# Kernel optimization log

Hardware: AMD Instinct MI355X
Metric: run time of the kernel (lower is better)

## Reference

```python
import jax, jax.numpy as jnp
import numpy as np
from jax import lax

B, H, W, CL, CC, CD, NH, NP = 8, 48, 48, 384, 384, 384, 12, 4
N = H * W
HD = CL // NH
SCALE = HD ** -0.5


def _pool_mat(n, out=7):
    # torch AdaptiveAvgPool2d bin edges: [floor(i*n/out), ceil((i+1)*n/out))
    M = np.zeros((out, n), np.float32)
    for i in range(out):
        s = (i * n) // out
        e = -(-((i + 1) * n) // out)
        M[i, s:e] = 1.0 / (e - s)
    return jnp.asarray(M)


def _resize_mat(out_n, in_n):
    # bilinear, align_corners=False (torch F.interpolate)
    M = np.zeros((out_n, in_n), np.float32)
    scale = in_n / out_n
    for o in range(out_n):
        src = (o + 0.5) * scale - 0.5
        src = min(max(src, 0.0), in_n - 1.0)
        i0 = int(np.floor(src))
        i1 = min(i0 + 1, in_n - 1)
        f = src - i0
        M[o, i0] += 1.0 - f
        M[o, i1] += f
    return jnp.asarray(M)


def _ln_c(x, g, b):
    # LayerNorm over channel dim of NCHW, eps=1e-6
    mu = jnp.mean(x, axis=1, keepdims=True)
    var = jnp.mean((x - mu) ** 2, axis=1, keepdims=True)
    xn = (x - mu) * lax.rsqrt(var + 1e-6)
    return xn * g[None, :, None, None] + b[None, :, None, None]


def _c1(x, w):
    # 1x1 conv, w: (out,in)
    return jnp.einsum('oc,bchw->bohw', w, x)


def _bilerp(feat, grid):
    # feat (G,C,Hs,Ws), grid (G,M,2) xy in [-1,1]; align_corners=False, zero padding
    G, C, Hs, Ws = feat.shape
    x = (grid[..., 0] + 1.0) * 0.5 * Ws - 0.5
    y = (grid[..., 1] + 1.0) * 0.5 * Hs - 0.5
    x0 = jnp.floor(x)
    y0 = jnp.floor(y)
    fx = x - x0
    fy = y - y0
    featf = feat.transpose(0, 2, 3, 1).reshape(G, Hs * Ws, C)
    x0i = x0.astype(jnp.int32)
    y0i = y0.astype(jnp.int32)

    def corner(ix, iy):
        valid = ((ix >= 0) & (ix < Ws) & (iy >= 0) & (iy < Hs)).astype(feat.dtype)
        flat = jnp.clip(iy, 0, Hs - 1) * Ws + jnp.clip(ix, 0, Ws - 1)
        g = jax.vmap(lambda f, i: f[i])(featf, flat)  # (G,M,C)
        return g * valid[..., None]

    v00 = corner(x0i, y0i)
    v01 = corner(x0i + 1, y0i)
    v10 = corner(x0i, y0i + 1)
    v11 = corner(x0i + 1, y0i + 1)
    w00 = ((1 - fx) * (1 - fy))[..., None]
    w01 = (fx * (1 - fy))[..., None]
    w10 = ((1 - fx) * fy)[..., None]
    w11 = (fx * fy)[..., None]
    return v00 * w00 + v01 * w01 + v10 * w10 + v11 * w11  # (G,M,C)


def _forward(local_feat, context_prior, deformable_x, W_q, W_k, W_v, W_pre, ln1_g, ln1_b,
             W_post, dw_w, dw_b, ln2_g, ln2_b, W_lo, b_lo, W_off, b_off,
             attention_biases, W_p, bn_g, bn_b, bn_mean, bn_var):
    q = _c1(local_feat, W_q)  # (B,CL,H,W)

    # context_offset_guide: 1x1 -> GELU -> adaptive pool 7x7 -> LN(C) -> 1x1 to 32 -> resize
    cg = jax.nn.gelu(_c1(context_prior, W_pre), approximate=False)
    Mh, Mw = _pool_mat(H), _pool_mat(W)
    pooled = jnp.einsum('oh,pw,bchw->bcop', Mh, Mw, cg)
    guide = _c1(_ln_c(pooled, ln1_g, ln1_b), W_post)  # (B,32,7,7)
    Uh, Uw = _resize_mat(H, 7), _resize_mat(W, 7)
    guide = jnp.einsum('Oh,Pw,bchw->bcOP', Uh, Uw, guide)  # (B,32,H,W)

    # local_offset_base: dwconv3x3 -> LN(C) -> GELU -> 1x1 to 32
    dw = lax.conv_general_dilated(local_feat, dw_w, (1, 1), [(1, 1), (1, 1)],
                                  dimension_numbers=('NCHW', 'OIHW', 'NCHW'),
                                  feature_group_count=CL) + dw_b[None, :, None, None]
    lo = jax.nn.gelu(_ln_c(dw, ln2_g, ln2_b), approximate=False)
    lo = _c1(lo, W_lo) + b_lo[None, :, None, None]  # (B,32,H,W)

    fused = jnp.concatenate([guide, lo], axis=1)  # (B,64,H,W)
    off = _c1(fused, W_off) + b_off[None, :, None, None]  # (B,NH*NP*2,H,W)
    off = off.transpose(0, 2, 3, 1).reshape(B, H, W, NH, NP, 2)
    offn = off / jnp.asarray([W, H], dtype=off.dtype)

    ry = (jnp.arange(H, dtype=off.dtype) + 0.5) / H
    rx = (jnp.arange(W, dtype=off.dtype) + 0.5) / W
    ref = jnp.stack([jnp.broadcast_to(rx[None, :], (H, W)),
                     jnp.broadcast_to(ry[:, None], (H, W))], axis=-1)  # (H,W,2) xy
    grid = (ref[None, :, :, None, None, :] + offn) * 2.0 - 1.0  # (B,H,W,NH,NP,2)

    gridh = grid.reshape(B, N, NH, NP, 2).transpose(0, 2, 1, 3, 4)  # (B,NH,N,NP,2)
    grid_r = gridh.reshape(B * NH, N * NP, 2)

    k = _c1(context_prior, W_k).reshape(B * NH, HD, H, W)
    v = _c1(deformable_x, W_v).reshape(B * NH, HD, H, W)
    k_s = _bilerp(k, grid_r).reshape(B, NH, N, NP, HD)
    v_s = _bilerp(v, grid_r).reshape(B, NH, N, NP, HD)

    qh = q.reshape(B, NH, HD, N).transpose(0, 1, 3, 2)  # (B,NH,N,HD)
    scores = jnp.einsum('bhnd,bhnpd->bhnp', qh, k_s) * SCALE

    # relative position bias: idx(p1,p2) = |dy|*W + |dx| (first-seen enumeration)
    px = jnp.clip(jnp.round((gridh[..., 0] + 1.0) * 0.5 * W - 0.5), 0, W - 1).astype(jnp.int32)
    py = jnp.clip(jnp.round((gridh[..., 1] + 1.0) * 0.5 * H - 0.5), 0, H - 1).astype(jnp.int32)
    n = jnp.arange(N, dtype=jnp.int32)
    qy = (n // W)[None, None, :, None]
    qx = (n % W)[None, None, :, None]
    bidx = jnp.abs(qy - py) * W + jnp.abs(qx - px)  # (B,NH,N,NP)
    bias = attention_biases[jnp.arange(NH)[None, :, None, None], bidx]

    attn = jax.nn.softmax(scores + bias, axis=-1)
    out = jnp.einsum('bhnp,bhnpd->bhnd', attn, v_s)  # (B,NH,N,HD)
    out = out.transpose(0, 1, 3, 2).reshape(B, CL, H, W)

    y = _c1(out, W_p)
    y = bn_g[None, :, None, None] * (y - bn_mean[None, :, None, None]) * \
        lax.rsqrt(bn_var[None, :, None, None] + 1e-5) + bn_b[None, :, None, None]
    return y


def setup_inputs():
    ks = jax.random.split(jax.random.key(0), 16)
    f32 = jnp.float32
    d = {
        'local_feat': jax.random.normal(ks[0], (B, CL, H, W), f32),
        'context_prior': jax.random.normal(ks[1], (B, CC, H, W), f32),
        'deformable_x': jax.random.normal(ks[2], (B, CD, H, W), f32),
        'W_q': jax.random.normal(ks[3], (CL, CL), f32) * 0.02,
        'W_k': jax.random.normal(ks[4], (CL, CC), f32) * 0.02,
        'W_v': jax.random.normal(ks[5], (CD, CD), f32) * 0.02,
        'W_pre': jax.random.normal(ks[6], (CC, CC), f32) * 0.02,
        'ln1_g': jnp.ones((CC,), f32),
        'ln1_b': jnp.zeros((CC,), f32),
        'W_post': jax.random.normal(ks[7], (32, CC), f32) * 0.02,
        'dw_w': jax.random.normal(ks[8], (CL, 1, 3, 3), f32) * 0.1,
        'dw_b': jnp.zeros((CL,), f32),
        'ln2_g': jnp.ones((CL,), f32),
        'ln2_b': jnp.zeros((CL,), f32),
        'W_lo': jax.random.normal(ks[9], (32, CL), f32) * 0.02,
        'b_lo': jnp.zeros((32,), f32),
        'W_off': jax.random.normal(ks[10], (NH * NP * 2, 64), f32) * 0.01,
        'b_off': jax.random.normal(ks[11], (NH * NP * 2,), f32) * 0.5,
        'attention_biases': jax.random.normal(ks[12], (NH, H * W), f32) * 0.02,
        'W_p': jax.random.normal(ks[13], (CL, CL), f32) * 0.02,
        'bn_g': jnp.ones((CL,), f32),
        'bn_b': jnp.zeros((CL,), f32),
        'bn_mean': jax.random.normal(ks[14], (CL,), f32) * 0.01,
        'bn_var': jax.random.uniform(ks[15], (CL,), f32, 0.5, 1.5),
    }
    return d


def reference(local_feat, context_prior, deformable_x, W_q, W_k, W_v, W_pre, ln1_g, ln1_b,
              W_post, dw_w, dw_b, ln2_g, ln2_b, W_lo, b_lo, W_off, b_off,
              attention_biases, W_p, bn_g, bn_b, bn_mean, bn_var):
    return _forward(local_feat, context_prior, deformable_x, W_q, W_k, W_v, W_pre, ln1_g,
                    ln1_b, W_post, dw_w, dw_b, ln2_g, ln2_b, W_lo, b_lo, W_off, b_off,
                    attention_biases, W_p, bn_g, bn_b, bn_mean, bn_var)
```

## Files before the change

kernel.cpp:

```cpp
#include <hip/hip_runtime.h>
#include <hip/hip_bf16.h>
#include <math.h>

#define B_ 8
#define H_ 48
#define W_ 48
#define N_ 2304
#define C_ 384
#define NH_ 12
#define NP_ 4
#define HD_ 32
#define SCALE_ 0.17677669529663687f

typedef unsigned short ushort;
typedef short bf16x8 __attribute__((ext_vector_type(8)));
typedef float f32x4 __attribute__((ext_vector_type(4)));

__device__ __forceinline__ float b2f(ushort u) {
    union { float f; unsigned i; } x; x.i = ((unsigned)u) << 16; return x.f;
}
__device__ __forceinline__ ushort f2b(float f) {
    __hip_bfloat16 h = __float2bfloat16(f);
    return *(ushort*)&h;
}
__device__ __forceinline__ float ldin(const void* p, size_t i, int isbf) {
    return isbf ? b2f(((const ushort*)p)[i]) : ((const float*)p)[i];
}
__device__ __forceinline__ float geluf(float x) {
    return 0.5f * x * (1.0f + erff(x * 0.70710678118654752440f));
}
__device__ __forceinline__ int iabs(int x) { return x < 0 ? -x : x; }

__device__ __forceinline__ void gl_lds16(const ushort* g, ushort* l) {
    __builtin_amdgcn_global_load_lds(
        (const __attribute__((address_space(1))) unsigned int*)g,
        (__attribute__((address_space(3))) unsigned int*)l, 16, 0, 0);
}

enum { EPI_NONE = 0, EPI_GELU = 1, EPI_BN = 3 };

__global__ void probe_kernel(const void* ones_ptr, int* flag) {
    if (threadIdx.x == 0 && blockIdx.x == 0)
        *flag = (*(const unsigned*)ones_ptr == 0x3F803F80u) ? 1 : 0;
}

#define PREP_MAX 24
struct PrepTab {
    const void* src[PREP_MAX];
    void*       dst[PREP_MAX];
    int         n[PREP_MAX];
    int         tobf[PREP_MAX];
};
__global__ __launch_bounds__(256) void prep_kernel(PrepTab tab, int ne, const int* __restrict__ dflag)
{
    const int isbf = *dflag;
    const int e = blockIdx.y;
    if (e >= ne) return;
    const int n = tab.n[e];
    const void* src = tab.src[e];
    if (tab.tobf[e]) {
        ushort* dst = (ushort*)tab.dst[e];
        if (isbf) {
            const ushort* s = (const ushort*)src;
            for (int i = blockIdx.x * 256 + threadIdx.x; i < n; i += gridDim.x * 256)
                dst[i] = s[i];
        } else {
            const float* s = (const float*)src;
            for (int i = blockIdx.x * 256 + threadIdx.x; i < n; i += gridDim.x * 256)
                dst[i] = f2b(s[i]);
        }
    } else {
        float* dst = (float*)tab.dst[e];
        if (isbf) {
            const ushort* s = (const ushort*)src;
            for (int i = blockIdx.x * 256 + threadIdx.x; i < n; i += gridDim.x * 256)
                dst[i] = b2f(s[i]);
        } else {
            const float* s = (const float*)src;
            for (int i = blockIdx.x * 256 + threadIdx.x; i < n; i += gridDim.x * 256)
                dst[i] = s[i];
        }
    }
}

__global__ void dwt_prep_kernel(const float* __restrict__ WdF, float* __restrict__ WdT)
{
    int c = threadIdx.x;
#pragma unroll
    for (int u = 0; u < 9; u++) WdT[u * C_ + c] = WdF[c * 9 + u];
}

struct TPtrs { const void* src[3]; ushort* dst[3]; };
__global__ __launch_bounds__(256) void transpose3_kernel(TPtrs tp, const int* __restrict__ dflag)
{
    const int isbf = *dflag;
    const int which = blockIdx.z >> 3;
    const int b = blockIdx.z & 7;
    const int n0 = blockIdx.x * 64, c0 = blockIdx.y * 32;
    const void* in = tp.src[which];
    ushort* out = tp.dst[which];
    const int t = threadIdx.x;

    __shared__ unsigned tile[64][33];

    if (isbf) {
        {
            const int c = t >> 3, s = t & 7;
            uint4 v = *(const uint4*)((const ushort*)in + ((size_t)b * C_ + c0 + c) * N_ + n0 + s * 8);
            const int nb = s * 8;
            tile[nb + 0][c] = v.x & 0xffff; tile[nb + 1][c] = v.x >> 16;
            tile[nb + 2][c] = v.y & 0xffff; tile[nb + 3][c] = v.y >> 16;
            tile[nb + 4][c] = v.z & 0xffff; tile[nb + 5][c] = v.z >> 16;
            tile[nb + 6][c] = v.w & 0xffff; tile[nb + 7][c] = v.w >> 16;
        }
        __syncthreads();
        {
            const int n = t >> 2, s = t & 3;
            const int cb = s * 8;
            unsigned p0 = tile[n][cb + 0] | (tile[n][cb + 1] << 16);
            unsigned p1 = tile[n][cb + 2] | (tile[n][cb + 3] << 16);
            unsigned p2 = tile[n][cb + 4] | (tile[n][cb + 5] << 16);
            unsigned p3 = tile[n][cb + 6] | (tile[n][cb + 7] << 16);
            uint4 o; o.x = p0; o.y = p1; o.z = p2; o.w = p3;
            *(uint4*)(out + ((size_t)b * N_ + n0 + n) * C_ + c0 + cb) = o;
        }
    } else {
        float* tf = (float*)&tile[0][0];
        const int tx = t & 31, ty = t >> 5;
        for (int sub = 0; sub < 2; sub++) {
            int ns = n0 + sub * 32;
            __syncthreads();
#pragma unroll
            for (int u = 0; u < 4; u++) {
                int c = ty + u * 8;
                tf[c * 33 + tx] = ((const float*)in)[((size_t)b * C_ + c0 + c) * N_ + ns + tx];
            }
            __syncthreads();
#pragma unroll
            for (int u = 0; u < 4; u++) {
                int n = ty + u * 8;
                out[((size_t)b * N_ + ns + n) * C_ + c0 + tx] = f2b(tf[tx * 33 + n]);
            }
        }
    }
}

template <int EPI, int OUTK>
__global__ __launch_bounds__(256) void gemm_mfma(
    const ushort* __restrict__ Ag, const ushort* __restrict__ Bg, void* __restrict__ Yg,
    int M, int NN, int K, size_t a_bs, size_t b_bs,
    const float* __restrict__ p0, const float* __restrict__ p1,
    const float* __restrict__ p2, const float* __restrict__ p3,
    const int* __restrict__ dflag)
{
    const int isbf = (OUTK == 2) ? *dflag : 1;
    __shared__ ushort As[128 * 32];
    __shared__ ushort Bs[128 * 32];
    const int tid = threadIdx.x;
    const int m0 = blockIdx.x * 128;
    const int n0 = blockIdx.y * 128;
    const int b  = blockIdx.z;
    const int lane = tid & 63, wave = tid >> 6;
    const int wr = wave >> 1, wc = wave & 1;
    const int quad = lane >> 4, l15 = lane & 15;

    f32x4 acc[4][4];
#pragma unroll
    for (int i = 0; i < 4; i++)
#pragma unroll
        for (int j = 0; j < 4; j++) acc[i][j] = (f32x4){0.f, 0.f, 0.f, 0.f};

    const size_t abase = (size_t)b * a_bs;
    const size_t bbase = (size_t)b * b_bs;

    for (int kc = 0; kc < K; kc += 32) {
#pragma unroll
        for (int u = 0; u < 2; u++) {
            int idx = tid + 256 * u;
            int r = idx >> 2, s = idx & 3;
            gl_lds16(Ag + abase + (size_t)(m0 + r) * K + kc + 8 * s, &As[idx * 8]);
            gl_lds16(Bg + bbase + (size_t)(n0 + r) * K + kc + 8 * s, &Bs[idx * 8]);
        }
        __syncthreads();
        bf16x8 af[4], bfr[4];
#pragma unroll
        for (int i = 0; i < 4; i++)
            af[i]  = *(const bf16x8*)&As[(wr * 64 + i * 16 + l15) * 32 + quad * 8];
#pragma unroll
        for (int j = 0; j < 4; j++)
            bfr[j] = *(const bf16x8*)&Bs[(wc * 64 + j * 16 + l15) * 32 + quad * 8];
#pragma unroll
        for (int i = 0; i < 4; i++)
#pragma unroll
            for (int j = 0; j < 4; j++)
                acc[i][j] = __builtin_amdgcn_mfma_f32_16x16x32_bf16(af[i], bfr[j], acc[i][j], 0, 0, 0);
        __syncthreads();
    }

    const size_t ybase = (size_t)b * (size_t)M * (size_t)NN;
#pragma unroll
    for (int i = 0; i < 4; i++) {
#pragma unroll
        for (int r = 0; r < 4; r++) {
            int m = m0 + wr * 64 + i * 16 + quad * 4 + r;
            float sc = 1.f, sh = 0.f;
            if (EPI == EPI_BN) {
                sc = p0[m] * rsqrtf(p3[m] + 1e-5f);
                sh = p1[m] - sc * p2[m];
            }
#pragma unroll
            for (int j = 0; j < 4; j++) {
                int nn = n0 + wc * 64 + j * 16 + l15;
                float v = acc[i][j][r];
                if (EPI == EPI_GELU) v = geluf(v);
                if (EPI == EPI_BN) v = sc * v + sh;
                size_t yi = ybase + (size_t)m * NN + nn;
                if (OUTK == 0) ((float*)Yg)[yi] = v;
                else if (OUTK == 1) ((ushort*)Yg)[yi] = f2b(v);
                else { if (isbf) ((ushort*)Yg)[yi] = f2b(v); else ((float*)Yg)[yi] = v; }
            }
        }
    }
}

struct QKVPtrs { const ushort* A[3]; const ushort* Bw[3]; ushort* Y[3]; };
__global__ __launch_bounds__(256) void gemm_qkv_kernel(QKVPtrs qp)
{
    const int which = blockIdx.z >> 3;
    const int b = blockIdx.z & 7;
    const ushort* Ag = qp.A[which];
    const ushort* Bg = qp.Bw[which];
    ushort* Yg = qp.Y[which];

    __shared__ ushort As[128 * 32];
    __shared__ ushort Bs[128 * 32];
    const int tid = threadIdx.x;
    const int m0 = blockIdx.x * 128;
    const int n0 = blockIdx.y * 128;
    const int lane = tid & 63, wave = tid >> 6;
    const int wr = wave >> 1, wc = wave & 1;
    const int quad = lane >> 4, l15 = lane & 15;

    f32x4 acc[4][4];
#pragma unroll
    for (int i = 0; i < 4; i++)
#pragma unroll
        for (int j = 0; j < 4; j++) acc[i][j] = (f32x4){0.f, 0.f, 0.f, 0.f};

    const size_t abase = (size_t)b * (size_t)N_ * C_;

    for (int kc = 0; kc < C_; kc += 32) {
#pragma unroll
        for (int u = 0; u < 2; u++) {
            int idx = tid + 256 * u;
            int r = idx >> 2, s = idx & 3;
            gl_lds16(Ag + abase + (size_t)(m0 + r) * C_ + kc + 8 * s, &As[idx * 8]);
            gl_lds16(Bg + (size_t)(n0 + r) * C_ + kc + 8 * s, &Bs[idx * 8]);
        }
        __syncthreads();
        bf16x8 af[4], bfr[4];
#pragma unroll
        for (int i = 0; i < 4; i++)
            af[i]  = *(const bf16x8*)&As[(wr * 64 + i * 16 + l15) * 32 + quad * 8];
#pragma unroll
        for (int j = 0; j < 4; j++)
            bfr[j] = *(const bf16x8*)&Bs[(wc * 64 + j * 16 + l15) * 32 + quad * 8];
#pragma unroll
        for (int i = 0; i < 4; i++)
#pragma unroll
            for (int j = 0; j < 4; j++)
                acc[i][j] = __builtin_amdgcn_mfma_f32_16x16x32_bf16(af[i], bfr[j], acc[i][j], 0, 0, 0);
        __syncthreads();
    }

    const size_t ybase = abase;
#pragma unroll
    for (int i = 0; i < 4; i++) {
#pragma unroll
        for (int r = 0; r < 4; r++) {
            int m = m0 + wr * 64 + i * 16 + quad * 4 + r;
#pragma unroll
            for (int j = 0; j < 4; j++) {
                int nn = n0 + wc * 64 + j * 16 + l15;
                Yg[ybase + (size_t)m * C_ + nn] = f2b(acc[i][j][r]);
            }
        }
    }
}

__global__ __launch_bounds__(384) void pool_ln_guide_kernel(
    const float* __restrict__ CG, const float* __restrict__ g, const float* __restrict__ bt,
    const ushort* __restrict__ WpostB, float* __restrict__ G7)
{
    const int cell = blockIdx.x % 49, b = blockIdx.x / 49;
    const int i = cell / 7, j = cell % 7, c = threadIdx.x;
    const int sh = (i * H_) / 7, eh = ((i + 1) * H_ + 6) / 7;
    const int sw = (j * W_) / 7, ew = ((j + 1) * W_ + 6) / 7;
    float s = 0.f;
    for (int h = sh; h < eh; h++)
        for (int w = sw; w < ew; w++)
            s += CG[((size_t)b * N_ + h * W_ + w) * C_ + c];
    s *= 1.0f / (float)((eh - sh) * (ew - sw));

    float rs = s, rq = s * s;
#pragma unroll
    for (int m = 1; m <= 32; m <<= 1) {
        rs += __shfl_xor(rs, m);
        rq += __shfl_xor(rq, m);
    }
    __shared__ float ss[6], sq[6], buf[C_];
    __shared__ float psum[12][33];
    int wid = threadIdx.x >> 6;
    if ((threadIdx.x & 63) == 0) { ss[wid] = rs; sq[wid] = rq; }
    __syncthreads();
    if (threadIdx.x == 0) {
        float ts = 0.f, tq = 0.f;
        for (int k = 0; k < 6; k++) { ts += ss[k]; tq += sq[k]; }
        ss[0] = ts; sq[0] = tq;
    }
    __syncthreads();
    float mu = ss[0] / (float)C_;
    float var = sq[0] / (float)C_ - mu * mu;
    float inv = rsqrtf(var + 1e-6f);
    buf[c] = (s - mu) * inv * g[c] + bt[c];
    __syncthreads();

    const int oc = threadIdx.x & 31, seg = threadIdx.x >> 5;
    const uint4* wp = (const uint4*)(WpostB + oc * C_ + seg * 32);
    float part = 0.f;
#pragma unroll
    for (int u = 0; u < 4; u++) {
        uint4 v = wp[u];
        const float* bb = &buf[seg * 32 + u * 8];
        part += b2f((ushort)(v.x & 0xffff)) * bb[0] + b2f((ushort)(v.x >> 16)) * bb[1];
        part += b2f((ushort)(v.y & 0xffff)) * bb[2] + b2f((ushort)(v.y >> 16)) * bb[3];
        part += b2f((ushort)(v.z & 0xffff)) * bb[4] + b2f((ushort)(v.z >> 16)) * bb[5];
        part += b2f((ushort)(v.w & 0xffff)) * bb[6] + b2f((ushort)(v.w >> 16)) * bb[7];
    }
    psum[seg][oc] = part;
    __syncthreads();
    if (threadIdx.x < 32) {
        float acc = 0.f;
#pragma unroll
        for (int k = 0; k < 12; k++) acc += psum[k][threadIdx.x];
        G7[((size_t)b * 49 + cell) * 32 + threadIdx.x] = acc;
    }
}

__global__ __launch_bounds__(384) void wcomb_prep_kernel(
    const ushort* __restrict__ WoffB, const ushort* __restrict__ WloB,
    const float* __restrict__ bloF, const float* __restrict__ boffF,
    ushort* __restrict__ Bext, float* __restrict__ biasp)
{
    const int co = blockIdx.x;
    const int c = threadIdx.x;
    float acc = 0.f;
#pragma unroll 8
    for (int j = 0; j < 32; j++)
        acc += b2f(WoffB[co * 64 + 32 + j]) * b2f(WloB[j * 384 + c]);
    ushort hi = f2b(acc);
    float r = acc - b2f(hi);
    ushort lo = f2b(r);
    Bext[co * 1152 + c] = hi;
    Bext[co * 1152 + 384 + c] = lo;
    Bext[co * 1152 + 768 + c] = hi;
    if (c == 0) {
        float bp = boffF[co];
        for (int j = 0; j < 32; j++)
            bp += b2f(WoffB[co * 64 + 32 + j]) * bloF[j];
        biasp[co] = bp;
    }
}

__global__ void og7_prep_kernel(
    const ushort* __restrict__ WoffB, const float* __restrict__ G7, float* __restrict__ OG7)
{
    const int bc = blockIdx.x;
    const int co = threadIdx.x;
    if (co >= 96) return;
    const float* g = G7 + (size_t)bc * 32;
    float acc = 0.f;
#pragma unroll 8
    for (int c = 0; c < 32; c++)
        acc += b2f(WoffB[co * 64 + c]) * g[c];
    OG7[(size_t)bc * 96 + co] = acc;
}

__global__ __launch_bounds__(512) void dw_ln_gelu_kernel(
    const ushort* __restrict__ LF, const float* __restrict__ WdT, const float* __restrict__ BdF,
    const float* __restrict__ g, const float* __restrict__ bt,
    ushort* __restrict__ AHI, ushort* __restrict__ ALO)
{
    const int wave = threadIdx.x >> 6, lane = threadIdx.x & 63;
    const int m = blockIdx.x * 8 + wave;
    const int b = m / N_, n = m % N_;
    const int h = n / W_, w = n % W_;
    const bool act = lane < 48;
    const int c0 = lane * 8;

    float acc[8];
#pragma unroll
    for (int j = 0; j < 8; j++) acc[j] = 0.f;
    if (act) {
        f32x4 b0 = *(const f32x4*)(BdF + c0);
        f32x4 b1 = *(const f32x4*)(BdF + c0 + 4);
#pragma unroll
        for (int j = 0; j < 4; j++) { acc[j] = b0[j]; acc[4 + j] = b1[j]; }
    }

#pragma unroll
    for (int u = 0; u < 9; u++) {
        const int ky = u / 3, kx = u % 3;
        const int y = h + ky - 1, x = w + kx - 1;
        if (act && y >= 0 && y < H_ && x >= 0 && x < W_) {
            uint4 v = *(const uint4*)(LF + ((size_t)b * N_ + y * W_ + x) * C_ + c0);
            f32x4 wa = *(const f32x4*)(WdT + u * C_ + c0);
            f32x4 wb = *(const f32x4*)(WdT + u * C_ + c0 + 4);
            acc[0] += wa[0] * b2f((ushort)(v.x & 0xffff));
            acc[1] += wa[1] * b2f((ushort)(v.x >> 16));
            acc[2] += wa[2] * b2f((ushort)(v.y & 0xffff));
            acc[3] += wa[3] * b2f((ushort)(v.y >> 16));
            acc[4] += wb[0] * b2f((ushort)(v.z & 0xffff));
            acc[5] += wb[1] * b2f((ushort)(v.z >> 16));
            acc[6] += wb[2] * b2f((ushort)(v.w & 0xffff));
            acc[7] += wb[3] * b2f((ushort)(v.w >> 16));
        }
    }

    float rs = 0.f, rq = 0.f;
#pragma unroll
    for (int j = 0; j < 8; j++) { rs += acc[j]; rq += acc[j] * acc[j]; }
#pragma unroll
    for (int s = 1; s <= 32; s <<= 1) {
        rs += __shfl_xor(rs, s);
        rq += __shfl_xor(rq, s);
    }
    float mu = rs / (float)C_;
    float var = rq / (float)C_ - mu * mu;
    float inv = rsqrtf(var + 1e-6f);

    if (act) {
        f32x4 g0 = *(const f32x4*)(g + c0);
        f32x4 g1 = *(const f32x4*)(g + c0 + 4);
        f32x4 t0 = *(const f32x4*)(bt + c0);
        f32x4 t1 = *(const f32x4*)(bt + c0 + 4);
        float v[8];
#pragma unroll
        for (int j = 0; j < 4; j++) {
            v[j]     = geluf((acc[j]     - mu) * inv * g0[j] + t0[j]);
            v[4 + j] = geluf((acc[4 + j] - mu) * inv * g1[j] + t1[j]);
        }
        uint4 hi, lo;
        ushort hs[8], ls[8];
#pragma unroll
        for (int j = 0; j < 8; j++) {
            hs[j] = f2b(v[j]);
            ls[j] = f2b(v[j] - b2f(hs[j]));
        }
        hi.x = (unsigned)hs[0] | ((unsigned)hs[1] << 16);
        hi.y = (unsigned)hs[2] | ((unsigned)hs[3] << 16);
        hi.z = (unsigned)hs[4] | ((unsigned)hs[5] << 16);
        hi.w = (unsigned)hs[6] | ((unsigned)hs[7] << 16);
        lo.x = (unsigned)ls[0] | ((unsigned)ls[1] << 16);
        lo.y = (unsigned)ls[2] | ((unsigned)ls[3] << 16);
        lo.z = (unsigned)ls[4] | ((unsigned)ls[5] << 16);
        lo.w = (unsigned)ls[6] | ((unsigned)ls[7] << 16);
        size_t idx = (size_t)m * C_ + c0;
        *(uint4*)(AHI + idx) = hi;
        *(uint4*)(ALO + idx) = lo;
    }
}

__global__ __launch_bounds__(256) void off_gemm_kernel(
    const ushort* __restrict__ AHI, const ushort* __restrict__ ALO,
    const ushort* __restrict__ Bext, const float* __restrict__ biasp,
    const float* __restrict__ OG7, float* __restrict__ OFF)
{
    __shared__ short As[128][40];
    __shared__ short Bs[96][40];
    const int tid = threadIdx.x;
    const int m0 = blockIdx.x * 128;
    const int lane = tid & 63, wave = tid >> 6;
    const int wr = wave >> 1, wc = wave & 1;
    const int quad = lane >> 4, l15 = lane & 15;

    f32x4 acc[4][3];
#pragma unroll
    for (int i = 0; i < 4; i++)
#pragma unroll
        for (int j = 0; j < 3; j++) acc[i][j] = (f32x4){0.f, 0.f, 0.f, 0.f};

    for (int kc = 0; kc < 1152; kc += 32) {
        const int seg = kc / 384;
        const int cc0 = kc - seg * 384;
        const ushort* Asrc = (seg < 2) ? AHI : ALO;
#pragma unroll
        for (int u = 0; u < 2; u++) {
            int idx = tid + 256 * u;
            int r = idx >> 2, s = idx & 3;
            *(uint4*)&As[r][s * 8] = *(const uint4*)(Asrc + (size_t)(m0 + r) * 384 + cc0 + 8 * s);
        }
        for (int i = tid; i < 384; i += 256) {
            int r = i >> 2, s = i & 3;
            *(uint4*)&Bs[r][s * 8] = *(const uint4*)(Bext + r * 1152 + kc + 8 * s);
        }
        __syncthreads();
        bf16x8 af[4], bfr[3];
#pragma unroll
        for (int i = 0; i < 4; i++) af[i]  = *(const bf16x8*)&As[wr * 64 + i * 16 + l15][quad * 8];
#pragma unroll
        for (int j = 0; j < 3; j++) bfr[j] = *(const bf16x8*)&Bs[wc * 48 + j * 16 + l15][quad * 8];
#pragma unroll
        for (int i = 0; i < 4; i++)
#pragma unroll
            for (int j = 0; j < 3; j++)
                acc[i][j] = __builtin_amdgcn_mfma_f32_16x16x32_bf16(af[i], bfr[j], acc[i][j], 0, 0, 0);
        __syncthreads();
    }

#pragma unroll
    for (int i = 0; i < 4; i++) {
#pragma unroll
        for (int r = 0; r < 4; r++) {
            int m = m0 + wr * 64 + i * 16 + quad * 4 + r;
            int b = m / N_, n = m - b * N_;
            int Pw = n % W_, Oh = n / W_;
            const float fs = 7.0f / 48.0f;
            float sy = fminf(fmaxf(((float)Oh + 0.5f) * fs - 0.5f, 0.f), 6.f);
            float sx = fminf(fmaxf(((float)Pw + 0.5f) * fs - 0.5f, 0.f), 6.f);
            int y0 = (int)floorf(sy), x0 = (int)floorf(sx);
            int y1 = min(y0 + 1, 6), x1 = min(x0 + 1, 6);
            float fy = sy - (float)y0, fx = sx - (float)x0;
            float w00 = (1.f - fy) * (1.f - fx), w01 = (1.f - fy) * fx;
            float w10 = fy * (1.f - fx), w11 = fy * fx;
            const float* ogb = OG7 + (size_t)b * 49 * 96;
            int c00 = (y0 * 7 + x0) * 96, c01 = (y0 * 7 + x1) * 96;
            int c10 = (y1 * 7 + x0) * 96, c11 = (y1 * 7 + x1) * 96;
#pragma unroll
            for (int j = 0; j < 3; j++) {
                int co = wc * 48 + j * 16 + l15;
                float v = acc[i][j][r] + biasp[co]
                        + w00 * ogb[c00 + co] + w01 * ogb[c01 + co]
                        + w10 * ogb[c10 + co] + w11 * ogb[c11 + co];
                OFF[(size_t)m * 96 + co] = v;
            }
        }
    }
}

__global__ __launch_bounds__(384) void attn_kernel(
    const ushort* __restrict__ Q, const ushort* __restrict__ K, const ushort* __restrict__ V,
    const float* __restrict__ OFF, const float* __restrict__ ABf, ushort* __restrict__ OUT)
{
    const int pairi = blockIdx.x;
    const int b = pairi / (N_ / 2);
    const int n0 = (pairi % (N_ / 2)) * 2;
    const int tid = threadIdx.x;

    __shared__ int   cidxS[96][4];
    __shared__ float cwS[96][4];
    __shared__ float biasS[96];

    if (tid < 96) {
        const int pos = tid / 48, idx = tid % 48;
        const int n = n0 + pos;
        const int h = n / W_, w = n % W_;
        const int nh = idx >> 2, p = idx & 3;
        const size_t ob = ((size_t)b * N_ + n) * 96 + nh * 8 + 2 * p;
        float ox = OFF[ob];
        float oy = OFF[ob + 1];
        float x = (float)w + ox;
        float y = (float)h + oy;

        int px = (int)fminf(fmaxf(rintf(x), 0.f), (float)(W_ - 1));
        int py = (int)fminf(fmaxf(rintf(y), 0.f), (float)(H_ - 1));
        biasS[tid] = ABf[(size_t)nh * N_ + iabs(h - py) * W_ + iabs(w - px)];

        float x0f = floorf(x), y0f = floorf(y);
        float fx = x - x0f, fy = y - y0f;
        int x0 = (int)x0f, y0 = (int)y0f;
#pragma unroll
        for (int cc = 0; cc < 4; cc++) {
            int dx = cc & 1, dy = cc >> 1;
            int ix = x0 + dx, iy = y0 + dy;
            bool valid = (ix >= 0) && (ix < W_) && (iy >= 0) && (iy < H_);
            int ixc = min(max(ix, 0), W_ - 1), iyc = min(max(iy, 0), H_ - 1);
            cidxS[tid][cc] = iyc * W_ + ixc;
            float wx = dx ? fx : (1.f - fx);
            float wy = dy ? fy : (1.f - fy);
            cwS[tid][cc] = valid ? wx * wy : 0.f;
        }
    }
    __syncthreads();

    const int pos = tid / 192, r = tid % 192;
    const int nh = r >> 4, dd = r & 15;
    const int n = n0 + pos;
    const size_t row = ((size_t)b * N_ + n) * C_ + nh * HD_ + dd * 2;
    unsigned qu = *(const unsigned*)(Q + row);
    const float q0 = b2f((ushort)(qu & 0xffff));
    const float q1 = b2f((ushort)(qu >> 16));
    const size_t kvbase = (size_t)b * N_ * C_ + nh * HD_ + dd * 2;
    const int s0 = pos * 48 + nh * 4;

    int   ci[NP_][4];
    float cw[NP_][4];
#pragma unroll
    for (int p = 0; p < NP_; p++)
#pragma unroll
        for (int cc = 0; cc < 4; cc++) {
            ci[p][cc] = cidxS[s0 + p][cc];
            cw[p][cc] = cwS[s0 + p][cc];
        }

    float sc[NP_];
#pragma unroll
    for (int p = 0; p < NP_; p++) {
        float ks0 = 0.f, ks1 = 0.f;
#pragma unroll
        for (int cc = 0; cc < 4; cc++) {
            unsigned kv = *(const unsigned*)(K + kvbase + (size_t)ci[p][cc] * C_);
            ks0 += cw[p][cc] * b2f((ushort)(kv & 0xffff));
            ks1 += cw[p][cc] * b2f((ushort)(kv >> 16));
        }
        float dot = q0 * ks0 + q1 * ks1;
#pragma unroll
        for (int m = 1; m <= 8; m <<= 1) dot += __shfl_xor(dot, m);
        sc[p] = dot * SCALE_ + biasS[s0 + p];
    }

    float m = fmaxf(fmaxf(sc[0], sc[1]), fmaxf(sc[2], sc[3]));
    float e[NP_], esum = 0.f;
#pragma unroll
    for (int p = 0; p < NP_; p++) { e[p] = __expf(sc[p] - m); esum += e[p]; }
    float inv = 1.0f / esum;

    float o0 = 0.f, o1 = 0.f;
#pragma unroll
    for (int p = 0; p < NP_; p++) {
        float vs0 = 0.f, vs1 = 0.f;
#pragma unroll
        for (int cc = 0; cc < 4; cc++) {
            unsigned vv = *(const unsigned*)(V + kvbase + (size_t)ci[p][cc] * C_);
            vs0 += cw[p][cc] * b2f((ushort)(vv & 0xffff));
            vs1 += cw[p][cc] * b2f((ushort)(vv >> 16));
        }
        float ep = e[p] * inv;
        o0 += ep * vs0;
        o1 += ep * vs1;
    }
    unsigned ou = (unsigned)f2b(o0) | ((unsigned)f2b(o1) << 16);
    *(unsigned*)(OUT + row) = ou;
}

extern "C" void kernel_launch(void* const* d_in, const int* in_sizes, int n_in,
                              void* d_out, int out_size, void* d_ws, size_t ws_size,
                              hipStream_t stream)
{
    const void* local_feat    = d_in[0];
    const void* context_prior = d_in[1];
    const void* deformable_x  = d_in[2];

    const size_t BIGE = (size_t)B_ * N_ * C_;

    char* wsb = (char*)d_ws;
    auto carve = [&](size_t bytes) { char* p = wsb; wsb += (bytes + 255) & ~(size_t)255; return p; };
    int*    flag = (int*)carve(256);
    ushort* T1   = (ushort*)carve(BIGE * 2);
    ushort* T2   = (ushort*)carve(BIGE * 2);
    ushort* T3   = (ushort*)carve(BIGE * 2);
    ushort* Qb   = (ushort*)carve(BIGE * 2);
    ushort* Kb   = (ushort*)carve(BIGE * 2);
    float*  CGR  = (float*)carve(BIGE * 4);
    float*  OFFB = (float*)carve((size_t)B_ * N_ * 96 * 4);
    float*  G7   = (float*)carve((size_t)B_ * 49 * 32 * 4);
    ushort* WqB   = (ushort*)carve(147456 * 2);
    ushort* WkB   = (ushort*)carve(147456 * 2);
    ushort* WvB   = (ushort*)carve(147456 * 2);
    ushort* WpreB = (ushort*)carve(147456 * 2);
    ushort* WpB   = (ushort*)carve(147456 * 2);
    ushort* WpostB= (ushort*)carve(12288 * 2);
    ushort* WloB  = (ushort*)carve(12288 * 2);
    ushort* WoffB = (ushort*)carve(6144 * 2);
    ushort* Bext  = (ushort*)carve(96 * 1152 * 2);
    float*  biasp = (float*)carve(96 * 4);
    float*  OG7   = (float*)carve((size_t)B_ * 49 * 96 * 4);
    float*  dwwF  = (float*)carve(3456 * 4);
    float*  dwwT  = (float*)carve(3456 * 4);
    float*  ABf   = (float*)carve(27648 * 4);
    float*  bloF  = (float*)carve(32 * 4);
    float*  boffF = (float*)carve(96 * 4);
    float*  dwbF  = (float*)carve(384 * 4);
    float*  ln1gF = (float*)carve(384 * 4);
    float*  ln1bF = (float*)carve(384 * 4);
    float*  ln2gF = (float*)carve(384 * 4);
    float*  ln2bF = (float*)carve(384 * 4);
    float*  bngF  = (float*)carve(384 * 4);
    float*  bnbF  = (float*)carve(384 * 4);
    float*  bnmF  = (float*)carve(384 * 4);
    float*  bnvF  = (float*)carve(384 * 4);
    ushort* Vb   = (ushort*)CGR;
    ushort* AOut = (ushort*)CGR + BIGE;
    ushort* AHI  = Qb;
    ushort* ALO  = Kb;

    probe_kernel<<<1, 64, 0, stream>>>(d_in[7] , flag);

    PrepTab tab;
    int ne = 0;
    auto add = [&](const void* s, void* d, int n, int tb) {
        tab.src[ne] = s; tab.dst[ne] = d; tab.n[ne] = n; tab.tobf[ne] = tb; ne++;
    };
    add(d_in[3],  WqB,   147456, 1);
    add(d_in[4],  WkB,   147456, 1);
    add(d_in[5],  WvB,   147456, 1);
    add(d_in[6],  WpreB, 147456, 1);
    add(d_in[19], WpB,   147456, 1);
    add(d_in[9],  WpostB, 12288, 1);
    add(d_in[14], WloB,   12288, 1);
    add(d_in[16], WoffB,   6144, 1);
    add(d_in[10], dwwF,    3456, 0);
    add(d_in[18], ABf,    27648, 0);
    add(d_in[15], bloF,      32, 0);
    add(d_in[17], boffF,     96, 0);
    add(d_in[11], dwbF,     384, 0);
    add(d_in[7],  ln1gF,    384, 0);
    add(d_in[8],  ln1bF,    384, 0);
    add(d_in[12], ln2gF,    384, 0);
    add(d_in[13], ln2bF,    384, 0);
    add(d_in[20], bngF,     384, 0);
    add(d_in[21], bnbF,     384, 0);
    add(d_in[22], bnmF,     384, 0);
    add(d_in[23], bnvF,     384, 0);
    prep_kernel<<<dim3(64, ne), 256, 0, stream>>>(tab, ne, flag);
    dwt_prep_kernel<<<1, 384, 0, stream>>>(dwwF, dwwT);

    dim3 blk256(256);
    dim3 t3grid(N_ / 64, C_ / 32, 3 * B_);
    dim3 ggrid(N_ / 128, C_ / 128, B_);
    dim3 qkvgrid(N_ / 128, C_ / 128, 3 * B_);
    dim3 fgrid(C_ / 128, N_ / 128, B_);
    const size_t BST = (size_t)N_ * C_;

    TPtrs tp;
    tp.src[0] = local_feat;    tp.dst[0] = T1;
    tp.src[1] = context_prior; tp.dst[1] = T2;
    tp.src[2] = deformable_x;  tp.dst[2] = T3;
    transpose3_kernel<<<t3grid, blk256, 0, stream>>>(tp, flag);

    wcomb_prep_kernel<<<96, 384, 0, stream>>>(WoffB, WloB, bloF, boffF, Bext, biasp);

    gemm_mfma<EPI_GELU, 0><<<ggrid, blk256, 0, stream>>>(
        T2, WpreB, CGR, N_, C_, C_, BST, 0, nullptr, nullptr, nullptr, nullptr, flag);
    pool_ln_guide_kernel<<<B_ * 49, 384, 0, stream>>>(CGR, ln1gF, ln1bF, WpostB, G7);
    og7_prep_kernel<<<B_ * 49, 96, 0, stream>>>(WoffB, G7, OG7);

    dw_ln_gelu_kernel<<<(B_ * N_) / 8, 512, 0, stream>>>(T1, dwwT, dwbF, ln2gF, ln2bF, AHI, ALO);

    off_gemm_kernel<<<(B_ * N_) / 128, blk256, 0, stream>>>(AHI, ALO, Bext, biasp, OG7, OFFB);

    QKVPtrs qp;
    qp.A[0] = T1; qp.Bw[0] = WqB; qp.Y[0] = Qb;
    qp.A[1] = T2; qp.Bw[1] = WkB; qp.Y[1] = Kb;
    qp.A[2] = T3; qp.Bw[2] = WvB; qp.Y[2] = Vb;
    gemm_qkv_kernel<<<qkvgrid, blk256, 0, stream>>>(qp);

    attn_kernel<<<(B_ * N_) / 2, 384, 0, stream>>>(Qb, Kb, Vb, OFFB, ABf, AOut);

    gemm_mfma<EPI_BN, 2><<<fgrid, blk256, 0, stream>>>(
        WpB, AOut, d_out, C_, N_, C_, 0, BST, bngF, bnbF, bnmF, bnvF, flag);
}
```

Measured before the change: 375.7 us.

## Merge pre-GELU GEMM into batched QKV GEMM launch and widen transpose tiles

The GELU pre-projection GEMM is folded into the Q/K/V batched GEMM as a fourth matrix in one launch, writing fp32 GELU output for that slot. Because Q, K and V are now produced before the other stages run, V, AHI and ALO get their own workspace buffers instead of aliasing Qb, Kb and CGR. The transpose kernel now handles 64x64 tiles per block rather than 64x32, halving the number of blocks. The aim is fewer launches and a larger grid that keeps more of the GPU busy. The cost is extra workspace memory and a branch on the output type inside the GEMM epilogue.

After: 382.5 us. No clear change (+1.8%).

```diff
diff --git a/kernel.cpp b/kernel.cpp
--- a/kernel.cpp
+++ b/kernel.cpp
@@ -96,16 +96,17 @@
     const int isbf = *dflag;
     const int which = blockIdx.z >> 3;
     const int b = blockIdx.z & 7;
-    const int n0 = blockIdx.x * 64, c0 = blockIdx.y * 32;
+    const int n0 = blockIdx.x * 64, c0 = blockIdx.y * 64;
     const void* in = tp.src[which];
     ushort* out = tp.dst[which];
     const int t = threadIdx.x;
 
-    __shared__ unsigned tile[64][33];
+    __shared__ unsigned tile[64][65];
 
     if (isbf) {
-        {
-            const int c = t >> 3, s = t & 7;
+#pragma unroll
+        for (int u = 0; u < 2; u++) {
+            const int c = (t >> 3) + 32 * u, s = t & 7;
             uint4 v = *(const uint4*)((const ushort*)in + ((size_t)b * C_ + c0 + c) * N_ + n0 + s * 8);
             const int nb = s * 8;
             tile[nb + 0][c] = v.x & 0xffff; tile[nb + 1][c] = v.x >> 16;
@@ -114,32 +115,33 @@
             tile[nb + 6][c] = v.w & 0xffff; tile[nb + 7][c] = v.w >> 16;
         }
         __syncthreads();
-        {
-            const int n = t >> 2, s = t & 3;
+#pragma unroll
+        for (int u = 0; u < 2; u++) {
+            const int n = (t >> 3) + 32 * u, s = t & 7;
             const int cb = s * 8;
-            unsigned p0 = tile[n][cb + 0] | (tile[n][cb + 1] << 16);
-            unsigned p1 = tile[n][cb + 2] | (tile[n][cb + 3] << 16);
-            unsigned p2 = tile[n][cb + 4] | (tile[n][cb + 5] << 16);
-            unsigned p3 = tile[n][cb + 6] | (tile[n][cb + 7] << 16);
-            uint4 o; o.x = p0; o.y = p1; o.z = p2; o.w = p3;
+            uint4 o;
+            o.x = tile[n][cb + 0] | (tile[n][cb + 1] << 16);
+            o.y = tile[n][cb + 2] | (tile[n][cb + 3] << 16);
+            o.z = tile[n][cb + 4] | (tile[n][cb + 5] << 16);
+            o.w = tile[n][cb + 6] | (tile[n][cb + 7] << 16);
             *(uint4*)(out + ((size_t)b * N_ + n0 + n) * C_ + c0 + cb) = o;
         }
     } else {
         float* tf = (float*)&tile[0][0];
         const int tx = t & 31, ty = t >> 5;
-        for (int sub = 0; sub < 2; sub++) {
-            int ns = n0 + sub * 32;
+        for (int sub = 0; sub < 4; sub++) {
+            int ns = n0 + (sub & 1) * 32, cs = c0 + (sub >> 1) * 32;
             __syncthreads();
 #pragma unroll
             for (int u = 0; u < 4; u++) {
                 int c = ty + u * 8;
-                tf[c * 33 + tx] = ((const float*)in)[((size_t)b * C_ + c0 + c) * N_ + ns + tx];
+                tf[c * 33 + tx] = ((const float*)in)[((size_t)b * C_ + cs + c) * N_ + ns + tx];
             }
             __syncthreads();
 #pragma unroll
             for (int u = 0; u < 4; u++) {
                 int n = ty + u * 8;
-                out[((size_t)b * N_ + ns + n) * C_ + c0 + tx] = f2b(tf[tx * 33 + n]);
+                out[((size_t)b * N_ + ns + n) * C_ + cs + tx] = f2b(tf[tx * 33 + n]);
             }
         }
     }
@@ -223,14 +225,14 @@
     }
 }
 
-struct QKVPtrs { const ushort* A[3]; const ushort* Bw[3]; ushort* Y[3]; };
-__global__ __launch_bounds__(256) void gemm_qkv_kernel(QKVPtrs qp)
+struct G4Ptrs { const ushort* A[4]; const ushort* Bw[4]; void* Y[4]; };
+__global__ __launch_bounds__(256) void gemm4_kernel(G4Ptrs qp)
 {
     const int which = blockIdx.z >> 3;
     const int b = blockIdx.z & 7;
     const ushort* Ag = qp.A[which];
     const ushort* Bg = qp.Bw[which];
-    ushort* Yg = qp.Y[which];
+    void* Yg = qp.Y[which];
 
     __shared__ ushort As[128 * 32];
     __shared__ ushort Bs[128 * 32];
@@ -273,7 +275,6 @@
         __syncthreads();
     }
 
-    const size_t ybase = abase;
 #pragma unroll
     for (int i = 0; i < 4; i++) {
 #pragma unroll
@@ -282,7 +283,9 @@
 #pragma unroll
             for (int j = 0; j < 4; j++) {
                 int nn = n0 + wc * 64 + j * 16 + l15;
-                Yg[ybase + (size_t)m * C_ + nn] = f2b(acc[i][j][r]);
+                size_t yi = abase + (size_t)m * C_ + nn;
+                if (which == 3) ((float*)Yg)[yi] = geluf(acc[i][j][r]);
+                else            ((ushort*)Yg)[yi] = f2b(acc[i][j][r]);
             }
         }
     }
@@ -671,6 +674,9 @@
     ushort* T3   = (ushort*)carve(BIGE * 2);
     ushort* Qb   = (ushort*)carve(BIGE * 2);
     ushort* Kb   = (ushort*)carve(BIGE * 2);
+    ushort* Vb   = (ushort*)carve(BIGE * 2);
+    ushort* AHI  = (ushort*)carve(BIGE * 2);
+    ushort* ALO  = (ushort*)carve(BIGE * 2);
     float*  CGR  = (float*)carve(BIGE * 4);
     float*  OFFB = (float*)carve((size_t)B_ * N_ * 96 * 4);
     float*  G7   = (float*)carve((size_t)B_ * 49 * 32 * 4);
@@ -699,10 +705,7 @@
     float*  bnbF  = (float*)carve(384 * 4);
     float*  bnmF  = (float*)carve(384 * 4);
     float*  bnvF  = (float*)carve(384 * 4);
-    ushort* Vb   = (ushort*)CGR;
-    ushort* AOut = (ushort*)CGR + BIGE;
-    ushort* AHI  = Qb;
-    ushort* ALO  = Kb;
+    ushort* AOut = (ushort*)CGR;
 
     probe_kernel<<<1, 64, 0, stream>>>(d_in[7] , flag);
 
@@ -736,9 +739,8 @@
     dwt_prep_kernel<<<1, 384, 0, stream>>>(dwwF, dwwT);
 
     dim3 blk256(256);
-    dim3 t3grid(N_ / 64, C_ / 32, 3 * B_);
-    dim3 ggrid(N_ / 128, C_ / 128, B_);
-    dim3 qkvgrid(N_ / 128, C_ / 128, 3 * B_);
+    dim3 t3grid(N_ / 64, C_ / 64, 3 * B_);
+    dim3 g4grid(N_ / 128, C_ / 128, 4 * B_);
     dim3 fgrid(C_ / 128, N_ / 128, B_);
     const size_t BST = (size_t)N_ * C_;
 
@@ -750,8 +752,13 @@
 
     wcomb_prep_kernel<<<96, 384, 0, stream>>>(WoffB, WloB, bloF, boffF, Bext, biasp);
 
-    gemm_mfma<EPI_GELU, 0><<<ggrid, blk256, 0, stream>>>(
-        T2, WpreB, CGR, N_, C_, C_, BST, 0, nullptr, nullptr, nullptr, nullptr, flag);
+    G4Ptrs qp;
+    qp.A[0] = T1; qp.Bw[0] = WqB;   qp.Y[0] = Qb;
+    qp.A[1] = T2; qp.Bw[1] = WkB;   qp.Y[1] = Kb;
+    qp.A[2] = T3; qp.Bw[2] = WvB;   qp.Y[2] = Vb;
+    qp.A[3] = T2; qp.Bw[3] = WpreB; qp.Y[3] = CGR;
+    gemm4_kernel<<<g4grid, blk256, 0, stream>>>(qp);
+
     pool_ln_guide_kernel<<<B_ * 49, 384, 0, stream>>>(CGR, ln1gF, ln1bF, WpostB, G7);
     og7_prep_kernel<<<B_ * 49, 96, 0, stream>>>(WoffB, G7, OG7);
 
@@ -759,12 +766,6 @@
 
     off_gemm_kernel<<<(B_ * N_) / 128, blk256, 0, stream>>>(AHI, ALO, Bext, biasp, OG7, OFFB);
 
-    QKVPtrs qp;
-    qp.A[0] = T1; qp.Bw[0] = WqB; qp.Y[0] = Qb;
-    qp.A[1] = T2; qp.Bw[1] = WkB; qp.Y[1] = Kb;
-    qp.A[2] = T3; qp.Bw[2] = WvB; qp.Y[2] = Vb;
-    gemm_qkv_kernel<<<qkvgrid, blk256, 0, stream>>>(qp);
-
     attn_kernel<<<(B_ * N_) / 2, 384, 0, stream>>>(Qb, Kb, Vb, OFFB, ABf, AOut);
 
     gemm_mfma<EPI_BN, 2><<<fgrid, blk256, 0, stream>>>(
```
